# Kernel tuning notes

Hardware: AMD Instinct MI355X
Metric: run time of the kernel (lower is better)

The kernel has to match this reference:

```python
import jax, jax.numpy as jnp
import numpy as np

N_USERS = 100000
N_ITEMS = 50000
N = N_USERS + N_ITEMS  # graph nodes
E = 2_400_000
B = 16384
EMB = 64
HID = 128
LN_EPS = 1e-5


def _gcn(x, W, b, src, dst):
    # PyG GCNConv (eval): sym-normalized aggregation with self-loops.
    xw = x @ W                                      # [N, out]
    deg = jnp.ones((N,), x.dtype).at[dst].add(1.0)  # in-degree + self-loop
    dinv = jax.lax.rsqrt(deg)
    norm = dinv[src] * dinv[dst]                    # [E]
    msg = xw[src] * norm[:, None]                   # [E, out] gather
    out = jax.ops.segment_sum(msg, dst, num_segments=N)
    out = out + xw * (dinv * dinv)[:, None]         # self-loop term (norm_ii = 1/deg_i)
    return out + b


def _ln(h, g, b):
    mu = jnp.mean(h, axis=-1, keepdims=True)
    var = jnp.mean(jnp.square(h - mu), axis=-1, keepdims=True)
    return (h - mu) * jax.lax.rsqrt(var + LN_EPS) * g + b


def setup_inputs() -> dict:
    key = jax.random.key(0)
    ks = jax.random.split(key, 20)
    f32 = jnp.float32
    def lin(k, fi, fo):
        return jax.random.normal(k, (fi, fo), f32) * (1.0 / np.sqrt(fi))
    inp = {
        "x": jax.random.normal(ks[0], (N, EMB), f32),
        "src": jax.random.randint(ks[1], (E,), 0, N, jnp.int32),
        "dst": jax.random.randint(ks[2], (E,), 0, N, jnp.int32),
        "user_indices": jax.random.randint(ks[3], (B,), 1, N_USERS + 1, jnp.int32),
        "item_indices": jax.random.randint(ks[4], (B,), 1, N_ITEMS + 1, jnp.int32),
        # GCNConv weights
        "W1": lin(ks[5], EMB, HID), "b1": jnp.zeros((HID,), f32),
        "W2": lin(ks[6], HID, EMB), "b2": jnp.zeros((EMB,), f32),
        # MLP head: Linear(128,128)-LN-ReLU-Linear(128,64)-LN-ReLU-Linear(64,1)
        "fcW1": lin(ks[7], 2 * EMB, HID), "fcb1": jnp.zeros((HID,), f32),
        "g1": jnp.ones((HID,), f32), "be1": jnp.zeros((HID,), f32),
        "fcW2": lin(ks[8], HID, HID // 2), "fcb2": jnp.zeros((HID // 2,), f32),
        "g2": jnp.ones((HID // 2,), f32), "be2": jnp.zeros((HID // 2,), f32),
        "fcW3": lin(ks[9], HID // 2, 1), "fcb3": jnp.zeros((1,), f32),
    }
    return inp


def reference(x, src, dst, user_indices, item_indices,
              W1, b1, W2, b2,
              fcW1, fcb1, g1, be1, fcW2, fcb2, g2, be2, fcW3, fcb3):
    # graph path (edge_index and x provided); dropout inactive in eval mode
    h = jax.nn.relu(_gcn(x, W1, b1, src, dst))
    h = _gcn(h, W2, b2, src, dst)                   # [N, EMB]
    user_emb = h[:N_USERS][user_indices - 1]        # [B, EMB]
    item_emb = h[N_USERS:][item_indices - 1]        # [B, EMB]
    c = jnp.concatenate([user_emb, item_emb], axis=1)  # [B, 2*EMB]
    z = jax.nn.relu(_ln(c @ fcW1 + fcb1, g1, be1))
    z = jax.nn.relu(_ln(z @ fcW2 + fcb2, g2, be2))
    z = z @ fcW3 + fcb3                             # [B, 1]
    return jax.nn.sigmoid(z).squeeze()
```

## Files before the change

### kernel.cpp

```cpp
#include <hip/hip_runtime.h>
#include <hip/hip_bf16.h>
#include <math.h>

#define N_USERS_C 100000
#define BK_SHIFT 9
#define BK_NODES 512

typedef __bf16 bf8_t __attribute__((ext_vector_type(8)));
typedef float f32x4 __attribute__((ext_vector_type(4)));

__device__ __forceinline__ unsigned int pack_bf16(float a, float b) {
    __hip_bfloat16 ha = __float2bfloat16(a), hb = __float2bfloat16(b);
    return ((unsigned int)(*(unsigned short*)&hb) << 16) | (unsigned int)(*(unsigned short*)&ha);
}
__device__ __forceinline__ unsigned short bf16_1(float a) {
    __hip_bfloat16 ha = __float2bfloat16(a);
    return *(unsigned short*)&ha;
}
__device__ __forceinline__ float bf_lo(unsigned int u) { return __uint_as_float(u << 16); }
__device__ __forceinline__ float bf_hi(unsigned int u) { return __uint_as_float(u & 0xffff0000u); }

__global__ __launch_bounds__(512) void k_pre(const int* __restrict__ dst, int* __restrict__ chist,
                                             const float* __restrict__ x, unsigned int* __restrict__ xb,
                                             int E, int nbk, int EB2, int n2) {
    __shared__ int lcnt[BK_NODES];
    const int bid = blockIdx.x;
    const int t = threadIdx.x;
    if (bid < EB2) {
        if (t < nbk) lcnt[t] = 0;
        __syncthreads();
        int e0 = bid * 4096;
        #pragma unroll
        for (int j = 0; j < 8; ++j) {
            int e = e0 + j * 512 + t;
            if (e < E) atomicAdd(&lcnt[dst[e] >> BK_SHIFT], 1);
        }
        __syncthreads();
        if (t < nbk && lcnt[t]) atomicAdd(&chist[t], lcnt[t]);
    } else {
        int base = (bid - EB2) * 2048;
        #pragma unroll
        for (int j = 0; j < 4; ++j) {
            int i = base + j * 512 + t;
            if (i < n2) {
                float2 v = ((const float2*)x)[i];
                xb[i] = pack_bf16(v.x, v.y);
            }
        }
    }
}

__global__ __launch_bounds__(512) void k_bin(const int* __restrict__ src,
                                             const int* __restrict__ dst,
                                             const int* __restrict__ chist,
                                             int* __restrict__ bcursor0,
                                             int* __restrict__ pairBuf, int E, int nbk) {
    __shared__ int lcnt[BK_NODES];
    __shared__ int lofs[BK_NODES];
    __shared__ int delta[BK_NODES];
    __shared__ int waveSum[8];
    __shared__ int sPack[4096];
    __shared__ unsigned short sBkt[4096];
    const int t = threadIdx.x;
    const int lane = t & 63;
    const int w = t >> 6;
    const int e0 = blockIdx.x * 4096;
    if (t < nbk) lcnt[t] = 0;
    __syncthreads();

    int mySrc[8], myB[8], myDl[8];
    #pragma unroll
    for (int j = 0; j < 8; ++j) {
        int e = e0 + j * 512 + t;
        if (e < E) {
            int sv = src[e], dv = dst[e];
            mySrc[j] = sv; myB[j] = dv >> BK_SHIFT; myDl[j] = dv & (BK_NODES - 1);
            atomicAdd(&lcnt[myB[j]], 1);
        } else myB[j] = -1;
    }
    __syncthreads();

    int v = (t < nbk) ? lcnt[t] : 0;
    int inc = v;
    #pragma unroll
    for (int off = 1; off < 64; off <<= 1) {
        int n = __shfl_up(inc, off);
        if (lane >= off) inc += n;
    }
    if (lane == 63) waveSum[w] = inc;
    int cv = (t < nbk) ? chist[t] : 0;
    int cinc = cv;
    #pragma unroll
    for (int off = 1; off < 64; off <<= 1) {
        int n = __shfl_up(cinc, off);
        if (lane >= off) cinc += n;
    }
    __shared__ int cWaveSum[8];
    if (lane == 63) cWaveSum[w] = cinc;
    __syncthreads();
    int wp = 0, cwp = 0;
    #pragma unroll
    for (int i = 0; i < 8; ++i) {
        wp += (i < w) ? waveSum[i] : 0;
        cwp += (i < w) ? cWaveSum[i] : 0;
    }
    int ex = wp + inc - v;
    int cbase = cwp + cinc - cv;
    if (t < nbk) {
        lofs[t] = ex;
        int gb = cbase + ((v > 0) ? atomicAdd(&bcursor0[t], v) : 0);
        delta[t] = gb - ex;
    }
    __syncthreads();

    #pragma unroll
    for (int j = 0; j < 8; ++j) {
        if (myB[j] >= 0) {
            int p = atomicAdd(&lofs[myB[j]], 1);
            sPack[p] = mySrc[j] | (myDl[j] << 18);
            sBkt[p] = (unsigned short)myB[j];
        }
    }
    __syncthreads();
    int total = (E - e0 < 4096) ? (E - e0) : 4096;
    for (int i = t; i < total; i += 512)
        pairBuf[delta[sBkt[i]] + i] = sPack[i];
}

__global__ __launch_bounds__(512) void k_bscatter(const int* __restrict__ pairBuf,
                                                  const int* __restrict__ chist,
                                                  int* __restrict__ rowstart,
                                                  float* __restrict__ dinv,
                                                  int* __restrict__ csr, int N, int E, int nbk) {
    const int b = blockIdx.x;
    const int n0 = b << BK_SHIFT;
    int nn = N - n0; if (nn > BK_NODES) nn = BK_NODES;
    __shared__ int hist[BK_NODES];
    __shared__ int curs[BK_NODES];
    __shared__ int waveSum[8];
    __shared__ int sE0, sE1;
    const int t = threadIdx.x;
    const int lane = t & 63;
    const int w = t >> 6;

    {
        int cv = (t < nbk) ? chist[t] : 0;
        int cinc = cv;
        #pragma unroll
        for (int off = 1; off < 64; off <<= 1) {
            int n = __shfl_up(cinc, off);
            if (lane >= off) cinc += n;
        }
        if (lane == 63) waveSum[w] = cinc;
        if (t < nn) hist[t] = 0;
        __syncthreads();
        int cwp = 0;
        #pragma unroll
        for (int i = 0; i < 8; ++i) cwp += (i < w) ? waveSum[i] : 0;
        if (t == b) { sE0 = cwp + cinc - cv; sE1 = cwp + cinc; }
    }
    __syncthreads();
    const int e0 = sE0, e1 = sE1;

    for (int e = e0 + t; e < e1; e += 512)
        atomicAdd(&hist[pairBuf[e] >> 18], 1);
    __syncthreads();

    int v = (t < nn) ? hist[t] : 0;
    int inc = v;
    #pragma unroll
    for (int off = 1; off < 64; off <<= 1) {
        int n = __shfl_up(inc, off);
        if (lane >= off) inc += n;
    }
    if (lane == 63) waveSum[w] = inc;
    __syncthreads();
    int wp = 0;
    #pragma unroll
    for (int i = 0; i < 8; ++i) wp += (i < w) ? waveSum[i] : 0;
    int ex = wp + inc - v;
    if (t < nn) {
        int r = e0 + ex;
        rowstart[n0 + t] = r;
        curs[t] = r;
        dinv[n0 + t] = rsqrtf((float)(v + 1));
    }
    if (b == gridDim.x - 1 && t == 0) rowstart[N] = E;
    __syncthreads();
    for (int e = e0 + t; e < e1; e += 512) {
        int pk = pairBuf[e];
        int pos = atomicAdd(&curs[pk >> 18], 1);
        csr[pos] = pk & 0x3FFFF;
    }
}

__global__ __launch_bounds__(256) void k_gather1(const int* __restrict__ rowstart,
                                                 const int* __restrict__ csr,
                                                 const float* __restrict__ dinv,
                                                 const uint4* __restrict__ xb4,
                                                 unsigned int* __restrict__ outb, int N) {
    const int node = blockIdx.x * 4 + (threadIdx.x >> 6);
    const int l = threadIdx.x & 63;
    if (node >= N) return;
    const int sub = l >> 3;
    const int c = l & 7;
    const int rs = rowstart[node];
    const int re = rowstart[node + 1];

    float acc[8] = {0.f, 0.f, 0.f, 0.f, 0.f, 0.f, 0.f, 0.f};
    for (int base = rs; base < re; base += 64) {
        int idx = base + l;
        int sE = (idx < re) ? csr[idx] : 0;
        float dE = (idx < re) ? dinv[sE] : 0.0f;
        int cnt = re - base; if (cnt > 64) cnt = 64;
        int groups = (cnt + 7) >> 3;
        for (int g = 0; g < groups; ++g) {
            int e = g * 8 + sub;
            int sk = __shfl(sE, e);
            float dk = __shfl(dE, e);
            uint4 u = xb4[(size_t)sk * 8 + c];
            acc[0] += dk * bf_lo(u.x); acc[1] += dk * bf_hi(u.x);
            acc[2] += dk * bf_lo(u.y); acc[3] += dk * bf_hi(u.y);
            acc[4] += dk * bf_lo(u.z); acc[5] += dk * bf_hi(u.z);
            acc[6] += dk * bf_lo(u.w); acc[7] += dk * bf_hi(u.w);
        }
    }
    #pragma unroll
    for (int m = 8; m < 64; m <<= 1)
        #pragma unroll
        for (int i = 0; i < 8; ++i) acc[i] += __shfl_xor(acc[i], m);
    if (sub == 0) {
        float dd = dinv[node];
        float d2 = dd * dd;
        uint4 us = xb4[(size_t)node * 8 + c];
        uint4 o;
        o.x = pack_bf16(dd * acc[0] + d2 * bf_lo(us.x), dd * acc[1] + d2 * bf_hi(us.x));
        o.y = pack_bf16(dd * acc[2] + d2 * bf_lo(us.y), dd * acc[3] + d2 * bf_hi(us.y));
        o.z = pack_bf16(dd * acc[4] + d2 * bf_lo(us.z), dd * acc[5] + d2 * bf_hi(us.z));
        o.w = pack_bf16(dd * acc[6] + d2 * bf_lo(us.w), dd * acc[7] + d2 * bf_hi(us.w));
        ((uint4*)outb)[(size_t)node * 8 + c] = o;
    }
}

__global__ __launch_bounds__(256) void k_layer12(const unsigned int* __restrict__ aggXb,
                                                 const float* __restrict__ W1,
                                                 const float* __restrict__ b1,
                                                 const float* __restrict__ W2,
                                                 const float* __restrict__ dinv,
                                                 unsigned int* __restrict__ xs2b, int N) {
    __shared__ unsigned int sA[64 * 36];
    __shared__ unsigned int sB[128 * 36];
    __shared__ unsigned int sC[64 * 68];
    const int t = threadIdx.x;
    const int w = t >> 6;
    const int l = t & 63;
    const int n16 = l & 15;
    const int quad = l >> 4;
    const int row0 = blockIdx.x * 64;

    for (int i = t; i < 512; i += 256) {
        int r = i >> 3, c = i & 7;
        int row = row0 + r;
        uint4 u = (row < N) ? ((const uint4*)aggXb)[(size_t)row * 8 + c]
                            : make_uint4(0u, 0u, 0u, 0u);
        *(uint4*)&sA[r * 36 + c * 4] = u;
    }
    for (int i = t; i < 4096; i += 256) {
        int kp = i >> 7, n = i & 127;
        float a0 = W1[(size_t)(2 * kp) * 128 + n];
        float a1 = W1[(size_t)(2 * kp + 1) * 128 + n];
        sB[n * 36 + kp] = pack_bf16(a0, a1);
    }
    __syncthreads();

    f32x4 acc[8];
    #pragma unroll
    for (int nt = 0; nt < 8; ++nt) acc[nt] = (f32x4){0.f, 0.f, 0.f, 0.f};
    {
        const int am = w * 16 + n16;
        bf8_t a0 = *(const bf8_t*)&sA[am * 36 + quad * 4];
        bf8_t a1 = *(const bf8_t*)&sA[am * 36 + 16 + quad * 4];
        #pragma unroll
        for (int nt = 0; nt < 8; ++nt) {
            bf8_t b0 = *(const bf8_t*)&sB[(nt * 16 + n16) * 36 + quad * 4];
            bf8_t b1v = *(const bf8_t*)&sB[(nt * 16 + n16) * 36 + 16 + quad * 4];
            acc[nt] = __builtin_amdgcn_mfma_f32_16x16x32_bf16(a0, b0, acc[nt], 0, 0, 0);
            acc[nt] = __builtin_amdgcn_mfma_f32_16x16x32_bf16(a1, b1v, acc[nt], 0, 0, 0);
        }
    }
    __syncthreads();

    {
        unsigned short* sC16 = (unsigned short*)sC;
        #pragma unroll
        for (int nt = 0; nt < 8; ++nt) {
            int col = nt * 16 + n16;
            float bv = b1[col];
            #pragma unroll
            for (int reg = 0; reg < 4; ++reg) {
                int r = w * 16 + quad * 4 + reg;
                sC16[r * 136 + col] = bf16_1(fmaxf(acc[nt][reg] + bv, 0.f));
            }
        }
    }
    for (int i = t; i < 4096; i += 256) {
        int kp = i >> 6, n = i & 63;
        float a0 = W2[(size_t)(2 * kp) * 64 + n];
        float a1 = W2[(size_t)(2 * kp + 1) * 64 + n];
        sB[n * 68 + kp] = pack_bf16(a0, a1);
    }
    __syncthreads();

    f32x4 acc2[4];
    #pragma unroll
    for (int nt = 0; nt < 4; ++nt) acc2[nt] = (f32x4){0.f, 0.f, 0.f, 0.f};
    {
        const int am = w * 16 + n16;
        #pragma unroll
        for (int ks = 0; ks < 4; ++ks) {
            bf8_t a = *(const bf8_t*)&sC[am * 68 + ks * 16 + quad * 4];
            #pragma unroll
            for (int nt = 0; nt < 4; ++nt) {
                bf8_t b = *(const bf8_t*)&sB[(nt * 16 + n16) * 68 + ks * 16 + quad * 4];
                acc2[nt] = __builtin_amdgcn_mfma_f32_16x16x32_bf16(a, b, acc2[nt], 0, 0, 0);
            }
        }
    }

    {
        unsigned short* sA16 = (unsigned short*)sA;
        #pragma unroll
        for (int reg = 0; reg < 4; ++reg) {
            int r = w * 16 + quad * 4 + reg;
            int row = row0 + r;
            float dd = (row < N) ? dinv[row] : 0.f;
            #pragma unroll
            for (int nt = 0; nt < 4; ++nt)
                sA16[r * 72 + nt * 16 + n16] = bf16_1(acc2[nt][reg] * dd);
        }
    }
    __syncthreads();
    for (int i = t; i < 512; i += 256) {
        int r = i >> 3, c = i & 7;
        int row = row0 + r;
        if (row < N)
            ((uint4*)xs2b)[(size_t)row * 8 + c] = *(uint4*)&sA[r * 36 + c * 4];
    }
}

__global__ __launch_bounds__(256) void k_gather_pairs(const int* __restrict__ rowstart,
                                                      const int* __restrict__ csr,
                                                      const float* __restrict__ dinv,
                                                      const uint4* __restrict__ xs2b4,
                                                      const float* __restrict__ b2,
                                                      const int* __restrict__ ui,
                                                      const int* __restrict__ ii,
                                                      float* __restrict__ cB, int B) {
    const int wave = threadIdx.x >> 6;
    const int b = blockIdx.x * 2 + (wave >> 1);
    const int half = wave & 1;
    const int l = threadIdx.x & 63;
    const int sub = l >> 3;
    const int c = l & 7;
    if (b >= B) return;
    const int node = (half == 0) ? (ui[b] - 1) : (N_USERS_C + ii[b] - 1);
    const int rs = rowstart[node];
    const int re = rowstart[node + 1];

    float acc[8] = {0.f, 0.f, 0.f, 0.f, 0.f, 0.f, 0.f, 0.f};
    for (int base = rs; base < re; base += 64) {
        int idx = base + l;
        int sE = (idx < re) ? csr[idx] : 0;
        float vE = (idx < re) ? 1.0f : 0.0f;
        int cnt = re - base; if (cnt > 64) cnt = 64;
        int groups = (cnt + 7) >> 3;
        for (int g = 0; g < groups; ++g) {
            int e = g * 8 + sub;
            int sk = __shfl(sE, e);
            float vk = __shfl(vE, e);
            uint4 u = xs2b4[(size_t)sk * 8 + c];
            acc[0] += vk * bf_lo(u.x); acc[1] += vk * bf_hi(u.x);
            acc[2] += vk * bf_lo(u.y); acc[3] += vk * bf_hi(u.y);
            acc[4] += vk * bf_lo(u.z); acc[5] += vk * bf_hi(u.z);
            acc[6] += vk * bf_lo(u.w); acc[7] += vk * bf_hi(u.w);
        }
    }
    #pragma unroll
    for (int m = 8; m < 64; m <<= 1)
        #pragma unroll
        for (int i = 0; i < 8; ++i) acc[i] += __shfl_xor(acc[i], m);
    if (sub == 0) {
        float dd = dinv[node];
        uint4 us = xs2b4[(size_t)node * 8 + c];
        float4 s0, s1;
        s0.x = bf_lo(us.x); s0.y = bf_hi(us.x); s0.z = bf_lo(us.y); s0.w = bf_hi(us.y);
        s1.x = bf_lo(us.z); s1.y = bf_hi(us.z); s1.z = bf_lo(us.w); s1.w = bf_hi(us.w);
        float4 bb0 = ((const float4*)b2)[c * 2];
        float4 bb1 = ((const float4*)b2)[c * 2 + 1];
        float4 o0, o1;
        o0.x = dd * (acc[0] + s0.x) + bb0.x;
        o0.y = dd * (acc[1] + s0.y) + bb0.y;
        o0.z = dd * (acc[2] + s0.z) + bb0.z;
        o0.w = dd * (acc[3] + s0.w) + bb0.w;
        o1.x = dd * (acc[4] + s1.x) + bb1.x;
        o1.y = dd * (acc[5] + s1.y) + bb1.y;
        o1.z = dd * (acc[6] + s1.z) + bb1.z;
        o1.w = dd * (acc[7] + s1.w) + bb1.w;
        ((float4*)cB)[(size_t)b * 32 + half * 16 + c * 2] = o0;
        ((float4*)cB)[(size_t)b * 32 + half * 16 + c * 2 + 1] = o1;
    }
}

__global__ __launch_bounds__(256) void k_mlp(const float* __restrict__ cB,
                                             const float* __restrict__ fcW1, const float* __restrict__ fcb1,
                                             const float* __restrict__ g1,   const float* __restrict__ be1,
                                             const float* __restrict__ fcW2, const float* __restrict__ fcb2,
                                             const float* __restrict__ g2,   const float* __restrict__ be2,
                                             const float* __restrict__ fcW3, const float* __restrict__ fcb3,
                                             float* __restrict__ out) {
    __shared__ float sIn[32 * 128];
    __shared__ float sW[64 * 128];
    const int t = threadIdx.x;
    const int row0 = blockIdx.x * 32;
    const int rg = t >> 4;
    const int cg = t & 15;

    for (int i = t; i < 1024; i += 256) {
        int r = i >> 5, c4 = i & 31;
        *(float4*)&sIn[r * 128 + c4 * 4] = *(const float4*)&cB[(size_t)(row0 + r) * 128 + c4 * 4];
    }

    float acc1[2][8];
    {
        float4 b01 = *(const float4*)&fcb1[cg * 8];
        float4 b23 = *(const float4*)&fcb1[cg * 8 + 4];
        #pragma unroll
        for (int jj = 0; jj < 2; ++jj) {
            acc1[jj][0] = b01.x; acc1[jj][1] = b01.y; acc1[jj][2] = b01.z; acc1[jj][3] = b01.w;
            acc1[jj][4] = b23.x; acc1[jj][5] = b23.y; acc1[jj][6] = b23.z; acc1[jj][7] = b23.w;
        }
    }
    for (int s = 0; s < 2; ++s) {
        __syncthreads();
        for (int i = t; i < 2048; i += 256) {
            int k = i >> 5, c4 = i & 31;
            *(float4*)&sW[k * 128 + c4 * 4] = *(const float4*)&fcW1[(size_t)(64 * s + k) * 128 + c4 * 4];
        }
        __syncthreads();
        for (int k0 = 0; k0 < 64; k0 += 4) {
            float4 a[2];
            #pragma unroll
            for (int jj = 0; jj < 2; ++jj)
                a[jj] = *(const float4*)&sIn[(rg * 2 + jj) * 128 + 64 * s + k0];
            #pragma unroll
            for (int kk = 0; kk < 4; ++kk) {
                float4 w0 = *(const float4*)&sW[(k0 + kk) * 128 + cg * 8];
                float4 w1 = *(const float4*)&sW[(k0 + kk) * 128 + cg * 8 + 4];
                #pragma unroll
                for (int jj = 0; jj < 2; ++jj) {
                    float f = ((const float*)&a[jj])[kk];
                    acc1[jj][0] += f * w0.x; acc1[jj][1] += f * w0.y;
                    acc1[jj][2] += f * w0.z; acc1[jj][3] += f * w0.w;
                    acc1[jj][4] += f * w1.x; acc1[jj][5] += f * w1.y;
                    acc1[jj][6] += f * w1.z; acc1[jj][7] += f * w1.w;
                }
            }
        }
    }
    __syncthreads();

    {
        float4 g01 = *(const float4*)&g1[cg * 8];
        float4 g23 = *(const float4*)&g1[cg * 8 + 4];
        float4 e01 = *(const float4*)&be1[cg * 8];
        float4 e23 = *(const float4*)&be1[cg * 8 + 4];
        float gv[8] = {g01.x, g01.y, g01.z, g01.w, g23.x, g23.y, g23.z, g23.w};
        float ev[8] = {e01.x, e01.y, e01.z, e01.w, e23.x, e23.y, e23.z, e23.w};
        #pragma unroll
        for (int jj = 0; jj < 2; ++jj) {
            float s_ = 0.f, ss = 0.f;
            #pragma unroll
            for (int c = 0; c < 8; ++c) { float v = acc1[jj][c]; s_ += v; ss += v * v; }
            #pragma unroll
            for (int m = 1; m < 16; m <<= 1) { s_ += __shfl_xor(s_, m); ss += __shfl_xor(ss, m); }
            float mu = s_ * (1.0f / 128.0f);
            float var = ss * (1.0f / 128.0f) - mu * mu;
            float rs = rsqrtf(var + 1e-5f);
            #pragma unroll
            for (int c = 0; c < 8; ++c) {
                float z = (acc1[jj][c] - mu) * rs * gv[c] + ev[c];
                sIn[(rg * 2 + jj) * 128 + cg * 8 + c] = fmaxf(z, 0.f);
            }
        }
    }
    __syncthreads();

    for (int i = t; i < 2048; i += 256) {
        int k = i >> 4, c4 = i & 15;
        *(float4*)&sW[k * 64 + c4 * 4] = *(const float4*)&fcW2[(size_t)k * 64 + c4 * 4];
    }
    float acc2[2][4];
    {
        float4 bv = *(const float4*)&fcb2[cg * 4];
        #pragma unroll
        for (int jj = 0; jj < 2; ++jj) {
            acc2[jj][0] = bv.x; acc2[jj][1] = bv.y; acc2[jj][2] = bv.z; acc2[jj][3] = bv.w;
        }
    }
    __syncthreads();
    for (int k0 = 0; k0 < 128; k0 += 4) {
        float4 a[2], w[4];
        #pragma unroll
        for (int jj = 0; jj < 2; ++jj) a[jj] = *(const float4*)&sIn[(rg * 2 + jj) * 128 + k0];
        #pragma unroll
        for (int kk = 0; kk < 4; ++kk) w[kk] = *(const float4*)&sW[(k0 + kk) * 64 + cg * 4];
        #pragma unroll
        for (int jj = 0; jj < 2; ++jj) {
            const float* aj = (const float*)&a[jj];
            #pragma unroll
            for (int kk = 0; kk < 4; ++kk) {
                float f = aj[kk];
                acc2[jj][0] += f * w[kk].x; acc2[jj][1] += f * w[kk].y;
                acc2[jj][2] += f * w[kk].z; acc2[jj][3] += f * w[kk].w;
            }
        }
    }

    {
        float4 gv4 = *(const float4*)&g2[cg * 4];
        float4 ev4 = *(const float4*)&be2[cg * 4];
        float4 w34 = *(const float4*)&fcW3[cg * 4];
        float gv[4] = {gv4.x, gv4.y, gv4.z, gv4.w};
        float ev[4] = {ev4.x, ev4.y, ev4.z, ev4.w};
        float wv[4] = {w34.x, w34.y, w34.z, w34.w};
        float b3 = fcb3[0];
        #pragma unroll
        for (int jj = 0; jj < 2; ++jj) {
            float s_ = 0.f, ss = 0.f;
            #pragma unroll
            for (int c = 0; c < 4; ++c) { float v = acc2[jj][c]; s_ += v; ss += v * v; }
            #pragma unroll
            for (int m = 1; m < 16; m <<= 1) { s_ += __shfl_xor(s_, m); ss += __shfl_xor(ss, m); }
            float mu = s_ * (1.0f / 64.0f);
            float var = ss * (1.0f / 64.0f) - mu * mu;
            float rs = rsqrtf(var + 1e-5f);
            float p = 0.f;
            #pragma unroll
            for (int c = 0; c < 4; ++c) {
                float z = fmaxf((acc2[jj][c] - mu) * rs * gv[c] + ev[c], 0.f);
                p += z * wv[c];
            }
            #pragma unroll
            for (int m = 1; m < 16; m <<= 1) p += __shfl_xor(p, m);
            if (cg == 0) out[row0 + rg * 2 + jj] = 1.0f / (1.0f + expf(-(p + b3)));
        }
    }
}

extern "C" void kernel_launch(void* const* d_in, const int* in_sizes, int n_in,
                              void* d_out, int out_size, void* d_ws, size_t ws_size,
                              hipStream_t stream) {
    const float* x    = (const float*)d_in[0];
    const int*   src  = (const int*)d_in[1];
    const int*   dst  = (const int*)d_in[2];
    const int*   ui   = (const int*)d_in[3];
    const int*   ii   = (const int*)d_in[4];
    const float* W1   = (const float*)d_in[5];
    const float* b1   = (const float*)d_in[6];
    const float* W2   = (const float*)d_in[7];
    const float* b2   = (const float*)d_in[8];
    const float* fcW1 = (const float*)d_in[9];
    const float* fcb1 = (const float*)d_in[10];
    const float* g1   = (const float*)d_in[11];
    const float* be1  = (const float*)d_in[12];
    const float* fcW2 = (const float*)d_in[13];
    const float* fcb2 = (const float*)d_in[14];
    const float* g2   = (const float*)d_in[15];
    const float* be2  = (const float*)d_in[16];
    const float* fcW3 = (const float*)d_in[17];
    const float* fcb3 = (const float*)d_in[18];
    float* out = (float*)d_out;

    const int N = in_sizes[0] / 64;
    const int E = in_sizes[1];
    const int B = in_sizes[3];
    const int NBK = (N + BK_NODES - 1) >> BK_SHIFT;
    const int EB2 = (E + 4095) / 4096;
    const int n2 = N * 32;
    const int XB = (n2 + 2047) / 2048;

    float* ws   = (float*)d_ws;
    float* dinv = ws;
    int* rowstart = (int*)(dinv + N);
    int* csr      = rowstart + (N + 1);
    unsigned int* xb = (unsigned int*)(csr + E);
    unsigned int* bufU = xb + (size_t)N * 32;
    unsigned int* xs2b = bufU + (size_t)N * 32;
    float* cB = (float*)(xs2b + (size_t)N * 32);
    int* pairBuf = (int*)bufU;
    int* chist   = pairBuf + E;
    int* bcursor = chist + 512;
    unsigned int* aggXb = bufU;

    hipMemsetAsync(chist, 0, 1024 * sizeof(int), stream);
    k_pre<<<EB2 + XB, 512, 0, stream>>>(dst, chist, x, xb, E, NBK, EB2, n2);
    k_bin<<<EB2, 512, 0, stream>>>(src, dst, chist, bcursor, pairBuf, E, NBK);
    k_bscatter<<<NBK, 512, 0, stream>>>(pairBuf, chist, rowstart, dinv, csr, N, E, NBK);

    k_gather1<<<(N + 3) / 4, 256, 0, stream>>>(rowstart, csr, dinv, (const uint4*)xb, aggXb, N);

    k_layer12<<<(N + 63) / 64, 256, 0, stream>>>(aggXb, W1, b1, W2, dinv, xs2b, N);

    k_gather_pairs<<<(B + 1) / 2, 256, 0, stream>>>(rowstart, csr, dinv, (const uint4*)xs2b,
                                                    b2, ui, ii, cB, B);

    k_mlp<<<B / 32, 256, 0, stream>>>(cB, fcW1, fcb1, g1, be1,
                                      fcW2, fcb2, g2, be2, fcW3, fcb3, out);
}
```

Baseline: 346.7 us.

## Fuse layer-1 neighbor gather into the dense layer-1/layer-2 MFMA kernel

Merges the per-node aggregation kernel into the kernel that applies W1, ReLU and W2. Each wave now gathers its 16 rows directly into shared memory instead of writing the aggregated bf16 features to global memory and reading them back, which removes one launch and a full N×64 round trip. In exchange, each block serializes 16 node gathers per wave, which may reduce memory-level parallelism compared with one node per wave across many blocks. The shared buffers are merged and a launch-bounds occupancy hint is added.

```diff
diff --git a/kernel.cpp b/kernel.cpp
--- a/kernel.cpp
+++ b/kernel.cpp
@@ -194,104 +194,95 @@
     }
 }
 
-__global__ __launch_bounds__(256) void k_gather1(const int* __restrict__ rowstart,
+__global__ __launch_bounds__(256, 4) void k_gl12(const int* __restrict__ rowstart,
                                                  const int* __restrict__ csr,
                                                  const float* __restrict__ dinv,
                                                  const uint4* __restrict__ xb4,
-                                                 unsigned int* __restrict__ outb, int N) {
-    const int node = blockIdx.x * 4 + (threadIdx.x >> 6);
-    const int l = threadIdx.x & 63;
-    if (node >= N) return;
-    const int sub = l >> 3;
-    const int c = l & 7;
-    const int rs = rowstart[node];
-    const int re = rowstart[node + 1];
-
-    float acc[8] = {0.f, 0.f, 0.f, 0.f, 0.f, 0.f, 0.f, 0.f};
-    for (int base = rs; base < re; base += 64) {
-        int idx = base + l;
-        int sE = (idx < re) ? csr[idx] : 0;
-        float dE = (idx < re) ? dinv[sE] : 0.0f;
-        int cnt = re - base; if (cnt > 64) cnt = 64;
-        int groups = (cnt + 7) >> 3;
-        for (int g = 0; g < groups; ++g) {
-            int e = g * 8 + sub;
-            int sk = __shfl(sE, e);
-            float dk = __shfl(dE, e);
-            uint4 u = xb4[(size_t)sk * 8 + c];
-            acc[0] += dk * bf_lo(u.x); acc[1] += dk * bf_hi(u.x);
-            acc[2] += dk * bf_lo(u.y); acc[3] += dk * bf_hi(u.y);
-            acc[4] += dk * bf_lo(u.z); acc[5] += dk * bf_hi(u.z);
-            acc[6] += dk * bf_lo(u.w); acc[7] += dk * bf_hi(u.w);
-        }
-    }
-    #pragma unroll
-    for (int m = 8; m < 64; m <<= 1)
-        #pragma unroll
-        for (int i = 0; i < 8; ++i) acc[i] += __shfl_xor(acc[i], m);
-    if (sub == 0) {
-        float dd = dinv[node];
-        float d2 = dd * dd;
-        uint4 us = xb4[(size_t)node * 8 + c];
-        uint4 o;
-        o.x = pack_bf16(dd * acc[0] + d2 * bf_lo(us.x), dd * acc[1] + d2 * bf_hi(us.x));
-        o.y = pack_bf16(dd * acc[2] + d2 * bf_lo(us.y), dd * acc[3] + d2 * bf_hi(us.y));
-        o.z = pack_bf16(dd * acc[4] + d2 * bf_lo(us.z), dd * acc[5] + d2 * bf_hi(us.z));
-        o.w = pack_bf16(dd * acc[6] + d2 * bf_lo(us.w), dd * acc[7] + d2 * bf_hi(us.w));
-        ((uint4*)outb)[(size_t)node * 8 + c] = o;
-    }
-}
-
-__global__ __launch_bounds__(256) void k_layer12(const unsigned int* __restrict__ aggXb,
                                                  const float* __restrict__ W1,
                                                  const float* __restrict__ b1,
                                                  const float* __restrict__ W2,
-                                                 const float* __restrict__ dinv,
                                                  unsigned int* __restrict__ xs2b, int N) {
-    __shared__ unsigned int sA[64 * 36];
+    __shared__ unsigned int sAC[64 * 68];
     __shared__ unsigned int sB[128 * 36];
-    __shared__ unsigned int sC[64 * 68];
     const int t = threadIdx.x;
     const int w = t >> 6;
     const int l = t & 63;
+    const int sub = l >> 3;
+    const int c = l & 7;
     const int n16 = l & 15;
     const int quad = l >> 4;
     const int row0 = blockIdx.x * 64;
 
-    for (int i = t; i < 512; i += 256) {
-        int r = i >> 3, c = i & 7;
-        int row = row0 + r;
-        uint4 u = (row < N) ? ((const uint4*)aggXb)[(size_t)row * 8 + c]
-                            : make_uint4(0u, 0u, 0u, 0u);
-        *(uint4*)&sA[r * 36 + c * 4] = u;
-    }
     for (int i = t; i < 4096; i += 256) {
         int kp = i >> 7, n = i & 127;
         float a0 = W1[(size_t)(2 * kp) * 128 + n];
         float a1 = W1[(size_t)(2 * kp + 1) * 128 + n];
         sB[n * 36 + kp] = pack_bf16(a0, a1);
     }
-    __syncthreads();
-
-    f32x4 acc[8];
-    #pragma unroll
-    for (int nt = 0; nt < 8; ++nt) acc[nt] = (f32x4){0.f, 0.f, 0.f, 0.f};
+
+    for (int r = w * 16; r < w * 16 + 16; ++r) {
+        const int node = row0 + r;
+        if (node < N) {
+            const int rs = rowstart[node];
+            const int re = rowstart[node + 1];
+            float acc[8] = {0.f, 0.f, 0.f, 0.f, 0.f, 0.f, 0.f, 0.f};
+            for (int base = rs; base < re; base += 64) {
+                int idx = base + l;
+                int sE = (idx < re) ? csr[idx] : 0;
+                float dE = (idx < re) ? dinv[sE] : 0.0f;
+                int cnt = re - base; if (cnt > 64) cnt = 64;
+                int groups = (cnt + 7) >> 3;
+                for (int g = 0; g < groups; ++g) {
+                    int e = g * 8 + sub;
+                    int sk = __shfl(sE, e);
+                    float dk = __shfl(dE, e);
+                    uint4 u = xb4[(size_t)sk * 8 + c];
+                    acc[0] += dk * bf_lo(u.x); acc[1] += dk * bf_hi(u.x);
+                    acc[2] += dk * bf_lo(u.y); acc[3] += dk * bf_hi(u.y);
+                    acc[4] += dk * bf_lo(u.z); acc[5] += dk * bf_hi(u.z);
+                    acc[6] += dk * bf_lo(u.w); acc[7] += dk * bf_hi(u.w);
+                }
+            }
+            #pragma unroll
+            for (int m = 8; m < 64; m <<= 1)
+                #pragma unroll
+                for (int i = 0; i < 8; ++i) acc[i] += __shfl_xor(acc[i], m);
+            if (sub == 0) {
+                float dd = dinv[node];
+                float d2 = dd * dd;
+                uint4 us = xb4[(size_t)node * 8 + c];
+                uint4 o;
+                o.x = pack_bf16(dd * acc[0] + d2 * bf_lo(us.x), dd * acc[1] + d2 * bf_hi(us.x));
+                o.y = pack_bf16(dd * acc[2] + d2 * bf_lo(us.y), dd * acc[3] + d2 * bf_hi(us.y));
+                o.z = pack_bf16(dd * acc[4] + d2 * bf_lo(us.z), dd * acc[5] + d2 * bf_hi(us.z));
+                o.w = pack_bf16(dd * acc[6] + d2 * bf_lo(us.w), dd * acc[7] + d2 * bf_hi(us.w));
+                *(uint4*)&sAC[r * 36 + c * 4] = o;
+            }
+        } else if (sub == 0) {
+            *(uint4*)&sAC[r * 36 + c * 4] = make_uint4(0u, 0u, 0u, 0u);
+        }
+    }
+    __syncthreads();
+
+    f32x4 acc1[8];
+    #pragma unroll
+    for (int nt = 0; nt < 8; ++nt) acc1[nt] = (f32x4){0.f, 0.f, 0.f, 0.f};
     {
         const int am = w * 16 + n16;
-        bf8_t a0 = *(const bf8_t*)&sA[am * 36 + quad * 4];
-        bf8_t a1 = *(const bf8_t*)&sA[am * 36 + 16 + quad * 4];
+        bf8_t a0 = *(const bf8_t*)&sAC[am * 36 + quad * 4];
+        bf8_t a1 = *(const bf8_t*)&sAC[am * 36 + 16 + quad * 4];
         #pragma unroll
         for (int nt = 0; nt < 8; ++nt) {
             bf8_t b0 = *(const bf8_t*)&sB[(nt * 16 + n16) * 36 + quad * 4];
             bf8_t b1v = *(const bf8_t*)&sB[(nt * 16 + n16) * 36 + 16 + quad * 4];
-            acc[nt] = __builtin_amdgcn_mfma_f32_16x16x32_bf16(a0, b0, acc[nt], 0, 0, 0);
-            acc[nt] = __builtin_amdgcn_mfma_f32_16x16x32_bf16(a1, b1v, acc[nt], 0, 0, 0);
-        }
-    }
-    __syncthreads();
-
-    {
-        unsigned short* sC16 = (unsigned short*)sC;
+            acc1[nt] = __builtin_amdgcn_mfma_f32_16x16x32_bf16(a0, b0, acc1[nt], 0, 0, 0);
+            acc1[nt] = __builtin_amdgcn_mfma_f32_16x16x32_bf16(a1, b1v, acc1[nt], 0, 0, 0);
+        }
+    }
+    __syncthreads();
+
+    {
+        unsigned short* sC16 = (unsigned short*)sAC;
         #pragma unroll
         for (int nt = 0; nt < 8; ++nt) {
             int col = nt * 16 + n16;
@@ -299,7 +290,7 @@
             #pragma unroll
             for (int reg = 0; reg < 4; ++reg) {
                 int r = w * 16 + quad * 4 + reg;
-                sC16[r * 136 + col] = bf16_1(fmaxf(acc[nt][reg] + bv, 0.f));
+                sC16[r * 136 + col] = bf16_1(fmaxf(acc1[nt][reg] + bv, 0.f));
             }
         }
     }
@@ -318,7 +309,7 @@
         const int am = w * 16 + n16;
         #pragma unroll
         for (int ks = 0; ks < 4; ++ks) {
-            bf8_t a = *(const bf8_t*)&sC[am * 68 + ks * 16 + quad * 4];
+            bf8_t a = *(const bf8_t*)&sAC[am * 68 + ks * 16 + quad * 4];
             #pragma unroll
             for (int nt = 0; nt < 4; ++nt) {
                 bf8_t b = *(const bf8_t*)&sB[(nt * 16 + n16) * 68 + ks * 16 + quad * 4];
@@ -326,9 +317,10 @@
             }
         }
     }
-
-    {
-        unsigned short* sA16 = (unsigned short*)sA;
+    __syncthreads();
+
+    {
+        unsigned short* sA16 = (unsigned short*)sAC;
         #pragma unroll
         for (int reg = 0; reg < 4; ++reg) {
             int r = w * 16 + quad * 4 + reg;
@@ -341,10 +333,10 @@
     }
     __syncthreads();
     for (int i = t; i < 512; i += 256) {
-        int r = i >> 3, c = i & 7;
+        int r = i >> 3, cc = i & 7;
         int row = row0 + r;
         if (row < N)
-            ((uint4*)xs2b)[(size_t)row * 8 + c] = *(uint4*)&sA[r * 36 + c * 4];
+            ((uint4*)xs2b)[(size_t)row * 8 + cc] = *(uint4*)&sAC[r * 36 + cc * 4];
     }
 }
 
@@ -600,16 +592,14 @@
     int* pairBuf = (int*)bufU;
     int* chist   = pairBuf + E;
     int* bcursor = chist + 512;
-    unsigned int* aggXb = bufU;
 
     hipMemsetAsync(chist, 0, 1024 * sizeof(int), stream);
     k_pre<<<EB2 + XB, 512, 0, stream>>>(dst, chist, x, xb, E, NBK, EB2, n2);
     k_bin<<<EB2, 512, 0, stream>>>(src, dst, chist, bcursor, pairBuf, E, NBK);
     k_bscatter<<<NBK, 512, 0, stream>>>(pairBuf, chist, rowstart, dinv, csr, N, E, NBK);
 
-    k_gather1<<<(N + 3) / 4, 256, 0, stream>>>(rowstart, csr, dinv, (const uint4*)xb, aggXb, N);
-
-    k_layer12<<<(N + 63) / 64, 256, 0, stream>>>(aggXb, W1, b1, W2, dinv, xs2b, N);
+    k_gl12<<<(N + 63) / 64, 256, 0, stream>>>(rowstart, csr, dinv, (const uint4*)xb,
+                                              W1, b1, W2, xs2b, N);
 
     k_gather_pairs<<<(B + 1) / 2, 256, 0, stream>>>(rowstart, csr, dinv, (const uint4*)xs2b,
                                                     b2, ui, ii, cB, B);
```

Result: slower. 377.6 us (+8.9%).
